# Kernel tuning notes

Measured on AMD Instinct MI355X. Metric: run time of the kernel, lower is better.

Reference implementation:

```python
import jax, jax.numpy as jnp
import numpy as np

C_IN = 128      # pair channel
C_HID = 32      # per-head hidden dim
H = 4           # heads
INF = 1e9
LN_EPS = 1e-5


def setup_inputs() -> dict:
    key = jax.random.key(0)
    ks = jax.random.split(key, 8)
    B, N = 1, 256
    s = 0.02
    return {
        "x": jax.random.normal(ks[0], (B, N, N, C_IN), dtype=jnp.float32),
        "mask": jnp.ones((B, N, N), dtype=jnp.float32),
        "ln_w": jnp.ones((C_IN,), dtype=jnp.float32),
        "ln_b": jnp.zeros((C_IN,), dtype=jnp.float32),
        "w_b": jax.random.normal(ks[1], (H, C_IN), dtype=jnp.float32) * s,      # triangle-bias linear (no bias)
        "w_q": jax.random.normal(ks[2], (H * C_HID, C_IN), dtype=jnp.float32) * s,
        "w_k": jax.random.normal(ks[3], (H * C_HID, C_IN), dtype=jnp.float32) * s,
        "w_v": jax.random.normal(ks[4], (H * C_HID, C_IN), dtype=jnp.float32) * s,
        "w_g": jax.random.normal(ks[5], (H * C_HID, C_IN), dtype=jnp.float32) * s,
        "b_g": jnp.ones((H * C_HID,), dtype=jnp.float32),
        "w_o": jax.random.normal(ks[6], (C_IN, H * C_HID), dtype=jnp.float32) * s,
        "b_o": jnp.zeros((C_IN,), dtype=jnp.float32),
    }


def reference(x, mask, ln_w, ln_b, w_b, w_q, w_k, w_v, w_g, b_g, w_o, b_o):
    # starting=True -> no transpose
    # LayerNorm over channel dim
    mu = jnp.mean(x, axis=-1, keepdims=True)
    var = jnp.var(x, axis=-1, keepdims=True)
    xn = (x - mu) * jax.lax.rsqrt(var + LN_EPS) * ln_w + ln_b            # [B,I,J,C]

    # mask bias: [B, I, 1, 1, J]
    mask_bias = (INF * (mask - 1.0))[..., :, None, None, :]

    # triangle bias: linear -> [B,I,J,H] -> permute -> [B,H,I,J] -> [B,1,H,I,J]
    tri_bias = jnp.einsum("bijc,hc->bhij", xn, w_b)[:, None]

    # QKV projections, per-head: weights reshaped to [H, D, C]
    Wq = w_q.reshape(H, C_HID, C_IN)
    Wk = w_k.reshape(H, C_HID, C_IN)
    Wv = w_v.reshape(H, C_HID, C_IN)
    scale = 1.0 / np.sqrt(C_HID)
    q = jnp.einsum("bijc,hdc->bihjd", xn, Wq) * scale                    # [B,I,H,J,D]
    k = jnp.einsum("bijc,hdc->bihjd", xn, Wk)
    v = jnp.einsum("bijc,hdc->bihjd", xn, Wv)

    # attention over the J (column) axis of each row i
    a = jnp.einsum("bihqd,bihkd->bihqk", q, k) + mask_bias + tri_bias    # [B,I,H,J,J]
    a = jax.nn.softmax(a, axis=-1)
    o = jnp.einsum("bihqk,bihkd->biqhd", a, v)                           # [B,I,J,H,D]

    # sigmoid gating
    g = jax.nn.sigmoid(jnp.einsum("bijc,ec->bije", xn, w_g) + b_g)       # [B,I,J,H*D]
    o = o.reshape(*o.shape[:-2], H * C_HID) * g

    # output projection
    return jnp.einsum("bije,ce->bijc", o, w_o) + b_o                     # [B,I,J,C_in]
```

## Files before the change

kernel.cpp:

```cpp
#include <hip/hip_runtime.h>

#define N 256
#define C 128
#define H 4
#define D 32
#define NP (N*N)
#define LN_EPS 1e-5f
#define LOG2E 1.4426950408889634f

using f32x4 = __attribute__((ext_vector_type(4))) float;
using bf8   = __attribute__((ext_vector_type(8))) short;

__device__ __forceinline__ float bf2f(ushort u) {
    union { uint u; float f; } v; v.u = ((uint)u) << 16; return v.f;
}
__device__ __forceinline__ ushort f2bf(float f) {
    union { float f; uint u; } v; v.f = f;
    uint u = v.u;
    u += 0x7fffu + ((u >> 16) & 1u);
    return (ushort)(u >> 16);
}
__device__ __forceinline__ ushort f2bf_trunc(float f) {
    union { float f; uint u; } v; v.f = f;
    return (ushort)(v.u >> 16);
}

__global__ __launch_bounds__(256) void prep_weights(
    const float* __restrict__ wq, const float* __restrict__ wk,
    const float* __restrict__ wv, const float* __restrict__ wg,
    const float* __restrict__ wb, const float* __restrict__ wo,
    ushort* __restrict__ Wcat, ushort* __restrict__ Wb, ushort* __restrict__ Wo)
{
    int t = blockIdx.x * 256 + threadIdx.x;
    const float scale = 0.17677669529663689f * LOG2E;
    float v;
    if (t < 16384)       v = wq[t] * scale;
    else if (t < 32768)  v = wk[t - 16384];
    else if (t < 49152)  v = wv[t - 32768];
    else                 v = wg[t - 49152];
    Wcat[t] = f2bf(v);
    if (t < 16384) Wo[t] = f2bf(wo[t]);
    if (t < 512)   Wb[t] = f2bf(wb[t]);
}

__global__ __launch_bounds__(256) void ln_kernel(
    const float* __restrict__ x, const float* __restrict__ lnw,
    const float* __restrict__ lnb, ushort* __restrict__ xn)
{
    int wave = threadIdx.x >> 6, lane = threadIdx.x & 63;
    int p = blockIdx.x * 4 + wave;
    const float* xp = x + (size_t)p * C;
    float a0 = xp[lane], a1 = xp[lane + 64];
    float s = a0 + a1, ss = a0 * a0 + a1 * a1;
    #pragma unroll
    for (int m = 1; m < 64; m <<= 1) {
        s  += __shfl_xor(s, m, 64);
        ss += __shfl_xor(ss, m, 64);
    }
    float mean = s * (1.f / 128.f);
    float var  = ss * (1.f / 128.f) - mean * mean;
    float rstd = rsqrtf(var + LN_EPS);
    ushort* op = xn + (size_t)p * C;
    op[lane]      = f2bf((a0 - mean) * rstd * lnw[lane]      + lnb[lane]);
    op[lane + 64] = f2bf((a1 - mean) * rstd * lnw[lane + 64] + lnb[lane + 64]);
}

__global__ __launch_bounds__(256) void tri_kernel(
    const ushort* __restrict__ xn, const ushort* __restrict__ Wb,
    ushort* __restrict__ tri_p)
{
    __shared__ float wb[512];
    int t = threadIdx.x;
    wb[t]       = bf2f(Wb[t]);
    wb[t + 256] = bf2f(Wb[t + 256]);
    __syncthreads();
    int p = blockIdx.x * 256 + t;
    const ushort* xp = xn + (size_t)p * C;
    float acc0 = 0, acc1 = 0, acc2 = 0, acc3 = 0;
    #pragma unroll
    for (int c8 = 0; c8 < 16; c8++) {
        uint4 pk = ((const uint4*)xp)[c8];
        const ushort* u = (const ushort*)&pk;
        #pragma unroll
        for (int j = 0; j < 8; j++) {
            float xv = bf2f(u[j]);
            int c = c8 * 8 + j;
            acc0 += xv * wb[c];
            acc1 += xv * wb[128 + c];
            acc2 += xv * wb[256 + c];
            acc3 += xv * wb[384 + c];
        }
    }
    int q = p >> 8, k = p & 255;
    int qc = q >> 4, quad = (q >> 2) & 3, r = q & 3;
    int n = k >> 4, lrow = k & 15;
    int lane = quad * 16 + lrow;
    int v = n * 4 + r, j = v >> 3, m = v & 7;
    int base = ((qc * 8 + j) * 64 + lane) * 8 + m;
    tri_p[base]             = f2bf(acc0 * LOG2E);
    tri_p[65536 + base]     = f2bf(acc1 * LOG2E);
    tri_p[2 * 65536 + base] = f2bf(acc2 * LOG2E);
    tri_p[3 * 65536 + base] = f2bf(acc3 * LOG2E);
}

__global__ __launch_bounds__(512, 4) void proj_gemm(
    const ushort* __restrict__ xn, const ushort* __restrict__ Wcat,
    const float* __restrict__ bg,
    ushort* __restrict__ qb, ushort* __restrict__ kb,
    ushort* __restrict__ vbT, ushort* __restrict__ gate)
{
    __shared__ ushort At[128 * 128];
    __shared__ ushort Bt[128 * 128];
    int mt = blockIdx.x;
    int nt = blockIdx.y;
    int t  = threadIdx.x;

    const uint4* Ag = (const uint4*)(xn   + (size_t)mt * 128 * C);
    const uint4* Bg = (const uint4*)(Wcat + (size_t)nt * 128 * C);
    #pragma unroll
    for (int ii = 0; ii < 4; ii++) {
        int idx = t + ii * 512;
        int row = idx >> 4, c8 = idx & 15;
        int sc = row * 16 + (c8 ^ (row & 7));
        ((uint4*)At)[sc] = Ag[idx];
        ((uint4*)Bt)[sc] = Bg[idx];
    }
    __syncthreads();

    int wave = t >> 6, lane = t & 63;
    int lrow = lane & 15, quad = lane >> 4;
    int wr = wave >> 1, wc = wave & 1;

    f32x4 acc[2][4];
    #pragma unroll
    for (int mi = 0; mi < 2; mi++)
        #pragma unroll
        for (int ni = 0; ni < 4; ni++) acc[mi][ni] = (f32x4){0.f, 0.f, 0.f, 0.f};

    #pragma unroll
    for (int ks = 0; ks < 4; ks++) {
        int c8 = ks * 4 + quad;
        bf8 a[2], b[4];
        #pragma unroll
        for (int mi = 0; mi < 2; mi++) {
            int row = wr * 32 + mi * 16 + lrow;
            a[mi] = *(const bf8*)&At[(row * 16 + (c8 ^ (row & 7))) * 8];
        }
        #pragma unroll
        for (int ni = 0; ni < 4; ni++) {
            int row = wc * 64 + ni * 16 + lrow;
            b[ni] = *(const bf8*)&Bt[(row * 16 + (c8 ^ (row & 7))) * 8];
        }
        #pragma unroll
        for (int mi = 0; mi < 2; mi++)
            #pragma unroll
            for (int ni = 0; ni < 4; ni++)
                acc[mi][ni] = __builtin_amdgcn_mfma_f32_16x16x32_bf16(a[mi], b[ni], acc[mi][ni], 0, 0, 0);
    }

    if (nt == 2) {
        __syncthreads();
        #pragma unroll
        for (int mi = 0; mi < 2; mi++) {
            #pragma unroll
            for (int ni = 0; ni < 4; ni++) {
                int col = wc * 64 + ni * 16 + lrow;
                #pragma unroll
                for (int r = 0; r < 4; r++) {
                    int keyl = wr * 32 + mi * 16 + quad * 4 + r;
                    Bt[col * 128 + (keyl ^ (lrow << 3))] = f2bf(acc[mi][ni][r]);
                }
            }
        }
        __syncthreads();
        int i_row = mt >> 1;
        #pragma unroll
        for (int itr = 0; itr < 4; itr++) {
            int oidx = itr * 512 + t;
            int col = oidx >> 4, kc = oidx & 15;
            bf8 val = *(const bf8*)&Bt[col * 128 + ((kc * 8) ^ ((col & 15) << 3))];
            *(bf8*)&vbT[(size_t)(i_row * 128 + col) * N + (mt & 1) * 128 + kc * 8] = val;
        }
    } else {
        ushort* dst = (nt == 0) ? qb : (nt == 1) ? kb : gate;
        bool gated = (nt == 3);
        #pragma unroll
        for (int mi = 0; mi < 2; mi++) {
            #pragma unroll
            for (int ni = 0; ni < 4; ni++) {
                int col = wc * 64 + ni * 16 + lrow;
                #pragma unroll
                for (int r = 0; r < 4; r++) {
                    int row = mt * 128 + wr * 32 + mi * 16 + quad * 4 + r;
                    float v = acc[mi][ni][r];
                    if (gated) v = 1.f / (1.f + __expf(-(v + bg[col])));
                    dst[(size_t)row * C + col] = f2bf(v);
                }
            }
        }
    }
}

__global__ __launch_bounds__(512, 4) void attn_kernel(
    const ushort* __restrict__ qb, const ushort* __restrict__ kb,
    const ushort* __restrict__ vbT, const ushort* __restrict__ tri_p,
    const float* __restrict__ mask, ushort* __restrict__ ob)
{
    __shared__ ushort Kf[8192];
    __shared__ ushort Vf[8192];
    __shared__ ushort Pf[8][2048];

    int i  = blockIdx.x;
    int h  = blockIdx.y;
    int t  = threadIdx.x;
    int wave = t >> 6, lane = t & 63;
    int lrow = lane & 15, quad = lane >> 4;

    {
        const ushort* kt = kb + (size_t)(i * N) * C + h * D;
        #pragma unroll
        for (int it = 0; it < 2; it++) {
            int idx = it * 512 + t;
            int key = idx >> 2, d0 = (idx & 3) * 8;
            bf8 kv = *(const bf8*)(kt + (size_t)key * C + d0);
            int c = (idx >> 6) * 64 + (idx & 3) * 16 + ((idx >> 2) & 15);
            *(bf8*)&Kf[c * 8] = kv;
        }
    }
    {
        const ushort* vt = vbT + (size_t)((i * H + h) * D) * N;
        #pragma unroll
        for (int it = 0; it < 2; it++) {
            int idx = it * 512 + t;
            bf8 vv = *(const bf8*)(vt + idx * 8);
            int c = (idx >> 9) * 512 + ((idx >> 2) & 7) * 64 + (idx & 3) * 16 + ((idx >> 5) & 15);
            c ^= (c >> 6) & 7;
            *(bf8*)&Vf[c * 8] = vv;
        }
    }
    float mb[16];
    #pragma unroll
    for (int n = 0; n < 16; n++)
        mb[n] = (1e9f * LOG2E) * (mask[i * N + n * 16 + lrow] - 1.0f);
    __syncthreads();

    ushort* Pw = &Pf[wave][0];
    const ushort* trih = tri_p + (size_t)h * 65536;
    int pq = quad * 32 + (lrow & 7);
    int l3 = (lrow >> 3) & 1;

    #pragma unroll 1
    for (int cc = 0; cc < 2; cc++) {
        int qc = wave * 2 + cc;
        bf8 aq = *(const bf8*)(qb + (size_t)(i * N + qc * 16 + lrow) * C + h * D + quad * 8);
        float sum[4] = {0.f, 0.f, 0.f, 0.f};
        f32x4 o[2];
        o[0] = (f32x4){0.f, 0.f, 0.f, 0.f};
        o[1] = (f32x4){0.f, 0.f, 0.f, 0.f};

        #pragma unroll
        for (int half = 0; half < 2; half++) {
            f32x4 s8[8];
            #pragma unroll
            for (int n8 = 0; n8 < 8; n8++) {
                bf8 kf = *(const bf8*)&Kf[((half * 8 + n8) * 64 + lane) * 8];
                s8[n8] = __builtin_amdgcn_mfma_f32_16x16x32_bf16(
                    aq, kf, (f32x4){0.f, 0.f, 0.f, 0.f}, 0, 0, 0);
            }
            const ushort* tp = trih + ((size_t)(qc * 8 + half * 4) * 64 + lane) * 8;
            bf8 tf[4];
            #pragma unroll
            for (int jj = 0; jj < 4; jj++)
                tf[jj] = *(const bf8*)(tp + jj * 512);

            #pragma unroll
            for (int n8 = 0; n8 < 8; n8++) {
                int pa = (n8 >> 1) * 512 + (((n8 << 1) + l3) & 3) * 128 + pq;
                #pragma unroll
                for (int r = 0; r < 4; r++) {
                    float tb = bf2f(((const ushort*)&tf[n8 >> 1])[((n8 & 1) << 2) + r]);
                    float e  = exp2f(s8[n8][r] + tb + mb[half * 8 + n8]);
                    sum[r]  += e;
                    Pw[pa + r * 8] = f2bf_trunc(e);
                }
            }
            __asm__ volatile("s_waitcnt lgkmcnt(0)" ::: "memory");

            #pragma unroll
            for (int ks = 0; ks < 4; ks++) {
                bf8 ap = *(const bf8*)&Pw[(ks * 64 + lane) * 8];
                int ksg = half * 4 + ks;
                #pragma unroll
                for (int nv = 0; nv < 2; nv++) {
                    int c = nv * 512 + ksg * 64 + (lane ^ (ksg & 7));
                    bf8 bv = *(const bf8*)&Vf[c * 8];
                    o[nv] = __builtin_amdgcn_mfma_f32_16x16x32_bf16(ap, bv, o[nv], 0, 0, 0);
                }
            }
        }
        #pragma unroll
        for (int r = 0; r < 4; r++) {
            float s = sum[r];
            s += __shfl_xor(s, 1, 64);
            s += __shfl_xor(s, 2, 64);
            s += __shfl_xor(s, 4, 64);
            s += __shfl_xor(s, 8, 64);
            sum[r] = 1.f / s;
        }
        #pragma unroll
        for (int nv = 0; nv < 2; nv++) {
            int d = nv * 16 + lrow;
            #pragma unroll
            for (int r = 0; r < 4; r++) {
                int qg = qc * 16 + quad * 4 + r;
                ob[(size_t)(i * N + qg) * C + h * D + d] = f2bf(o[nv][r] * sum[r]);
            }
        }
    }
}

__global__ __launch_bounds__(512, 4) void out_gemm(
    const ushort* __restrict__ ob, const ushort* __restrict__ gate,
    const ushort* __restrict__ Wo, const float* __restrict__ bo,
    float* __restrict__ out)
{
    __shared__ ushort At[128 * 128];
    __shared__ ushort Bt[128 * 128];
    int mt = blockIdx.x;
    int t  = threadIdx.x;

    const uint4* Og = (const uint4*)(ob   + (size_t)mt * 128 * C);
    const uint4* Gg = (const uint4*)(gate + (size_t)mt * 128 * C);
    const uint4* Bg = (const uint4*)Wo;
    #pragma unroll
    for (int ii = 0; ii < 4; ii++) {
        int idx = t + ii * 512;
        int row = idx >> 4, c8 = idx & 15;
        int sc = row * 16 + (c8 ^ (row & 7));
        uint4 o4 = Og[idx], g4 = Gg[idx], r4;
        const ushort* os = (const ushort*)&o4;
        const ushort* gs = (const ushort*)&g4;
        ushort* rs = (ushort*)&r4;
        #pragma unroll
        for (int j = 0; j < 8; j++) rs[j] = f2bf(bf2f(os[j]) * bf2f(gs[j]));
        ((uint4*)At)[sc] = r4;
        ((uint4*)Bt)[sc] = Bg[idx];
    }
    __syncthreads();

    int wave = t >> 6, lane = t & 63;
    int lrow = lane & 15, quad = lane >> 4;
    int wr = wave >> 1, wc = wave & 1;

    f32x4 acc[2][4];
    #pragma unroll
    for (int mi = 0; mi < 2; mi++)
        #pragma unroll
        for (int ni = 0; ni < 4; ni++) acc[mi][ni] = (f32x4){0.f, 0.f, 0.f, 0.f};

    #pragma unroll
    for (int ks = 0; ks < 4; ks++) {
        int c8 = ks * 4 + quad;
        bf8 a[2], b[4];
        #pragma unroll
        for (int mi = 0; mi < 2; mi++) {
            int row = wr * 32 + mi * 16 + lrow;
            a[mi] = *(const bf8*)&At[(row * 16 + (c8 ^ (row & 7))) * 8];
        }
        #pragma unroll
        for (int ni = 0; ni < 4; ni++) {
            int row = wc * 64 + ni * 16 + lrow;
            b[ni] = *(const bf8*)&Bt[(row * 16 + (c8 ^ (row & 7))) * 8];
        }
        #pragma unroll
        for (int mi = 0; mi < 2; mi++)
            #pragma unroll
            for (int ni = 0; ni < 4; ni++)
                acc[mi][ni] = __builtin_amdgcn_mfma_f32_16x16x32_bf16(a[mi], b[ni], acc[mi][ni], 0, 0, 0);
    }

    #pragma unroll
    for (int mi = 0; mi < 2; mi++) {
        #pragma unroll
        for (int ni = 0; ni < 4; ni++) {
            int col = wc * 64 + ni * 16 + lrow;
            float bias = bo[col];
            #pragma unroll
            for (int r = 0; r < 4; r++) {
                int row = mt * 128 + wr * 32 + mi * 16 + quad * 4 + r;
                out[(size_t)row * C + col] = acc[mi][ni][r] + bias;
            }
        }
    }
}

extern "C" void kernel_launch(void* const* d_in, const int* in_sizes, int n_in,
                              void* d_out, int out_size, void* d_ws, size_t ws_size,
                              hipStream_t stream)
{
    const float* x    = (const float*)d_in[0];
    const float* mask = (const float*)d_in[1];
    const float* lnw  = (const float*)d_in[2];
    const float* lnb  = (const float*)d_in[3];
    const float* wb   = (const float*)d_in[4];
    const float* wq   = (const float*)d_in[5];
    const float* wk   = (const float*)d_in[6];
    const float* wv   = (const float*)d_in[7];
    const float* wg   = (const float*)d_in[8];
    const float* bg   = (const float*)d_in[9];
    const float* wo   = (const float*)d_in[10];
    const float* bo   = (const float*)d_in[11];
    float* out = (float*)d_out;

    uintptr_t w = (uintptr_t)d_ws;
    ushort* xn    = (ushort*)w; w += (size_t)NP * C * 2;
    ushort* qb    = (ushort*)w; w += (size_t)NP * C * 2;
    ushort* kb    = (ushort*)w; w += (size_t)NP * C * 2;
    ushort* vbT   = (ushort*)w; w += (size_t)NP * C * 2;
    ushort* gate  = (ushort*)w; w += (size_t)NP * C * 2;
    ushort* ob    = (ushort*)w; w += (size_t)NP * C * 2;
    ushort* tri_p = (ushort*)w; w += (size_t)H * NP * 2;
    ushort* Wcat  = (ushort*)w; w += 512 * 128 * 2;
    ushort* Wb    = (ushort*)w; w += 512 * 2;
    ushort* Wo    = (ushort*)w; w += 128 * 128 * 2;

    prep_weights<<<256, 256, 0, stream>>>(wq, wk, wv, wg, wb, wo, Wcat, Wb, Wo);
    ln_kernel<<<NP / 4, 256, 0, stream>>>(x, lnw, lnb, xn);
    tri_kernel<<<NP / 256, 256, 0, stream>>>(xn, Wb, tri_p);
    proj_gemm<<<dim3(NP / 128, 4), 512, 0, stream>>>(xn, Wcat, bg, qb, kb, vbT, gate);
    attn_kernel<<<dim3(N, H), 512, 0, stream>>>(qb, kb, vbT, tri_p, mask, ob);
    out_gemm<<<NP / 128, 512, 0, stream>>>(ob, gate, Wo, bo, out);
}
```

Baseline: 181.7 us.

## Fuse LayerNorm into tri-bias and projection GEMM kernels, drop xn buffer

Removes the standalone LayerNorm and triangle-bias kernels and the bf16 xn intermediate. One kernel recomputes LayerNorm and produces the tri bias with a wave reduction. The projection GEMM now recomputes LayerNorm from fp32 x into shared memory and loops over all four weight tiles per block, so the A tile is reused instead of being reloaded by four blocks. In exchange, x is read twice in fp32 instead of once plus a bf16 reread, the grid shrinks from 2048 to 512 blocks, and the four N tiles run serially inside each block.

```diff
diff --git a/kernel.cpp b/kernel.cpp
--- a/kernel.cpp
+++ b/kernel.cpp
@@ -28,8 +28,8 @@
 __global__ __launch_bounds__(256) void prep_weights(
     const float* __restrict__ wq, const float* __restrict__ wk,
     const float* __restrict__ wv, const float* __restrict__ wg,
-    const float* __restrict__ wb, const float* __restrict__ wo,
-    ushort* __restrict__ Wcat, ushort* __restrict__ Wb, ushort* __restrict__ Wo)
+    const float* __restrict__ wo,
+    ushort* __restrict__ Wcat, ushort* __restrict__ Wo)
 {
     int t = blockIdx.x * 256 + threadIdx.x;
     const float scale = 0.17677669529663689f * LOG2E;
@@ -40,12 +40,12 @@
     else                 v = wg[t - 49152];
     Wcat[t] = f2bf(v);
     if (t < 16384) Wo[t] = f2bf(wo[t]);
-    if (t < 512)   Wb[t] = f2bf(wb[t]);
-}
-
-__global__ __launch_bounds__(256) void ln_kernel(
+}
+
+__global__ __launch_bounds__(256) void ln_tri_kernel(
     const float* __restrict__ x, const float* __restrict__ lnw,
-    const float* __restrict__ lnb, ushort* __restrict__ xn)
+    const float* __restrict__ lnb, const float* __restrict__ wb,
+    ushort* __restrict__ tri_p)
 {
     int wave = threadIdx.x >> 6, lane = threadIdx.x & 63;
     int p = blockIdx.x * 4 + wave;
@@ -60,51 +60,34 @@
     float mean = s * (1.f / 128.f);
     float var  = ss * (1.f / 128.f) - mean * mean;
     float rstd = rsqrtf(var + LN_EPS);
-    ushort* op = xn + (size_t)p * C;
-    op[lane]      = f2bf((a0 - mean) * rstd * lnw[lane]      + lnb[lane]);
-    op[lane + 64] = f2bf((a1 - mean) * rstd * lnw[lane + 64] + lnb[lane + 64]);
-}
-
-__global__ __launch_bounds__(256) void tri_kernel(
-    const ushort* __restrict__ xn, const ushort* __restrict__ Wb,
-    ushort* __restrict__ tri_p)
-{
-    __shared__ float wb[512];
-    int t = threadIdx.x;
-    wb[t]       = bf2f(Wb[t]);
-    wb[t + 256] = bf2f(Wb[t + 256]);
-    __syncthreads();
-    int p = blockIdx.x * 256 + t;
-    const ushort* xp = xn + (size_t)p * C;
-    float acc0 = 0, acc1 = 0, acc2 = 0, acc3 = 0;
-    #pragma unroll
-    for (int c8 = 0; c8 < 16; c8++) {
-        uint4 pk = ((const uint4*)xp)[c8];
-        const ushort* u = (const ushort*)&pk;
-        #pragma unroll
-        for (int j = 0; j < 8; j++) {
-            float xv = bf2f(u[j]);
-            int c = c8 * 8 + j;
-            acc0 += xv * wb[c];
-            acc1 += xv * wb[128 + c];
-            acc2 += xv * wb[256 + c];
-            acc3 += xv * wb[384 + c];
-        }
-    }
-    int q = p >> 8, k = p & 255;
-    int qc = q >> 4, quad = (q >> 2) & 3, r = q & 3;
-    int n = k >> 4, lrow = k & 15;
-    int lane = quad * 16 + lrow;
-    int v = n * 4 + r, j = v >> 3, m = v & 7;
-    int base = ((qc * 8 + j) * 64 + lane) * 8 + m;
-    tri_p[base]             = f2bf(acc0 * LOG2E);
-    tri_p[65536 + base]     = f2bf(acc1 * LOG2E);
-    tri_p[2 * 65536 + base] = f2bf(acc2 * LOG2E);
-    tri_p[3 * 65536 + base] = f2bf(acc3 * LOG2E);
-}
-
-__global__ __launch_bounds__(512, 4) void proj_gemm(
-    const ushort* __restrict__ xn, const ushort* __restrict__ Wcat,
+    float v0 = (a0 - mean) * rstd * lnw[lane]      + lnb[lane];
+    float v1 = (a1 - mean) * rstd * lnw[lane + 64] + lnb[lane + 64];
+
+    float t[H];
+    #pragma unroll
+    for (int h = 0; h < H; h++)
+        t[h] = v0 * wb[h * C + lane] + v1 * wb[h * C + 64 + lane];
+    #pragma unroll
+    for (int m = 1; m < 64; m <<= 1) {
+        #pragma unroll
+        for (int h = 0; h < H; h++) t[h] += __shfl_xor(t[h], m, 64);
+    }
+    if (lane == 0) {
+        int q = p >> 8, k = p & 255;
+        int qc = q >> 4, quad = (q >> 2) & 3, r = q & 3;
+        int n = k >> 4, lrow = k & 15;
+        int ln2 = quad * 16 + lrow;
+        int v = n * 4 + r, j = v >> 3, m = v & 7;
+        int base = ((qc * 8 + j) * 64 + ln2) * 8 + m;
+        #pragma unroll
+        for (int h = 0; h < H; h++)
+            tri_p[h * 65536 + base] = f2bf(t[h] * LOG2E);
+    }
+}
+
+__global__ __launch_bounds__(512, 4) void proj_ln_gemm(
+    const float* __restrict__ x, const float* __restrict__ lnw,
+    const float* __restrict__ lnb, const ushort* __restrict__ Wcat,
     const float* __restrict__ bg,
     ushort* __restrict__ qb, ushort* __restrict__ kb,
     ushort* __restrict__ vbT, ushort* __restrict__ gate)
@@ -112,89 +95,123 @@
     __shared__ ushort At[128 * 128];
     __shared__ ushort Bt[128 * 128];
     int mt = blockIdx.x;
-    int nt = blockIdx.y;
     int t  = threadIdx.x;
 
-    const uint4* Ag = (const uint4*)(xn   + (size_t)mt * 128 * C);
-    const uint4* Bg = (const uint4*)(Wcat + (size_t)nt * 128 * C);
     #pragma unroll
     for (int ii = 0; ii < 4; ii++) {
         int idx = t + ii * 512;
         int row = idx >> 4, c8 = idx & 15;
-        int sc = row * 16 + (c8 ^ (row & 7));
-        ((uint4*)At)[sc] = Ag[idx];
-        ((uint4*)Bt)[sc] = Bg[idx];
-    }
-    __syncthreads();
+        const float* xr = x + ((size_t)(mt * 128 + row)) * C + c8 * 8;
+        float4 f0 = ((const float4*)xr)[0];
+        float4 f1 = ((const float4*)xr)[1];
+        float s  = f0.x + f0.y + f0.z + f0.w + f1.x + f1.y + f1.z + f1.w;
+        float ss = f0.x*f0.x + f0.y*f0.y + f0.z*f0.z + f0.w*f0.w
+                 + f1.x*f1.x + f1.y*f1.y + f1.z*f1.z + f1.w*f1.w;
+        #pragma unroll
+        for (int m = 1; m < 16; m <<= 1) {
+            s  += __shfl_xor(s, m, 64);
+            ss += __shfl_xor(ss, m, 64);
+        }
+        float mean = s * (1.f / 128.f);
+        float var  = ss * (1.f / 128.f) - mean * mean;
+        float rstd = rsqrtf(var + LN_EPS);
+        float4 w0 = ((const float4*)(lnw + c8 * 8))[0];
+        float4 w1 = ((const float4*)(lnw + c8 * 8))[1];
+        float4 b0 = ((const float4*)(lnb + c8 * 8))[0];
+        float4 b1 = ((const float4*)(lnb + c8 * 8))[1];
+        union { ushort us[8]; uint4 v; } r;
+        r.us[0] = f2bf((f0.x - mean) * rstd * w0.x + b0.x);
+        r.us[1] = f2bf((f0.y - mean) * rstd * w0.y + b0.y);
+        r.us[2] = f2bf((f0.z - mean) * rstd * w0.z + b0.z);
+        r.us[3] = f2bf((f0.w - mean) * rstd * w0.w + b0.w);
+        r.us[4] = f2bf((f1.x - mean) * rstd * w1.x + b1.x);
+        r.us[5] = f2bf((f1.y - mean) * rstd * w1.y + b1.y);
+        r.us[6] = f2bf((f1.z - mean) * rstd * w1.z + b1.z);
+        r.us[7] = f2bf((f1.w - mean) * rstd * w1.w + b1.w);
+        ((uint4*)At)[row * 16 + (c8 ^ (row & 7))] = r.v;
+    }
 
     int wave = t >> 6, lane = t & 63;
     int lrow = lane & 15, quad = lane >> 4;
     int wr = wave >> 1, wc = wave & 1;
-
-    f32x4 acc[2][4];
-    #pragma unroll
-    for (int mi = 0; mi < 2; mi++)
-        #pragma unroll
-        for (int ni = 0; ni < 4; ni++) acc[mi][ni] = (f32x4){0.f, 0.f, 0.f, 0.f};
-
-    #pragma unroll
-    for (int ks = 0; ks < 4; ks++) {
-        int c8 = ks * 4 + quad;
-        bf8 a[2], b[4];
-        #pragma unroll
-        for (int mi = 0; mi < 2; mi++) {
-            int row = wr * 32 + mi * 16 + lrow;
-            a[mi] = *(const bf8*)&At[(row * 16 + (c8 ^ (row & 7))) * 8];
-        }
-        #pragma unroll
-        for (int ni = 0; ni < 4; ni++) {
-            int row = wc * 64 + ni * 16 + lrow;
-            b[ni] = *(const bf8*)&Bt[(row * 16 + (c8 ^ (row & 7))) * 8];
-        }
+    int i_row = mt >> 1;
+
+    #pragma unroll 1
+    for (int nt = 0; nt < 4; nt++) {
+        __syncthreads();
+        const uint4* Bg = (const uint4*)(Wcat + (size_t)nt * 128 * C);
+        #pragma unroll
+        for (int ii = 0; ii < 4; ii++) {
+            int idx = t + ii * 512;
+            int row = idx >> 4, c8 = idx & 15;
+            ((uint4*)Bt)[row * 16 + (c8 ^ (row & 7))] = Bg[idx];
+        }
+        __syncthreads();
+
+        f32x4 acc[2][4];
         #pragma unroll
         for (int mi = 0; mi < 2; mi++)
             #pragma unroll
-            for (int ni = 0; ni < 4; ni++)
-                acc[mi][ni] = __builtin_amdgcn_mfma_f32_16x16x32_bf16(a[mi], b[ni], acc[mi][ni], 0, 0, 0);
-    }
-
-    if (nt == 2) {
-        __syncthreads();
-        #pragma unroll
-        for (int mi = 0; mi < 2; mi++) {
+            for (int ni = 0; ni < 4; ni++) acc[mi][ni] = (f32x4){0.f, 0.f, 0.f, 0.f};
+
+        #pragma unroll
+        for (int ks = 0; ks < 4; ks++) {
+            int c8 = ks * 4 + quad;
+            bf8 a[2], b[4];
+            #pragma unroll
+            for (int mi = 0; mi < 2; mi++) {
+                int row = wr * 32 + mi * 16 + lrow;
+                a[mi] = *(const bf8*)&At[(row * 16 + (c8 ^ (row & 7))) * 8];
+            }
             #pragma unroll
             for (int ni = 0; ni < 4; ni++) {
-                int col = wc * 64 + ni * 16 + lrow;
+                int row = wc * 64 + ni * 16 + lrow;
+                b[ni] = *(const bf8*)&Bt[(row * 16 + (c8 ^ (row & 7))) * 8];
+            }
+            #pragma unroll
+            for (int mi = 0; mi < 2; mi++)
                 #pragma unroll
-                for (int r = 0; r < 4; r++) {
-                    int keyl = wr * 32 + mi * 16 + quad * 4 + r;
-                    Bt[col * 128 + (keyl ^ (lrow << 3))] = f2bf(acc[mi][ni][r]);
+                for (int ni = 0; ni < 4; ni++)
+                    acc[mi][ni] = __builtin_amdgcn_mfma_f32_16x16x32_bf16(a[mi], b[ni], acc[mi][ni], 0, 0, 0);
+        }
+
+        if (nt == 2) {
+            __syncthreads();
+            #pragma unroll
+            for (int mi = 0; mi < 2; mi++) {
+                #pragma unroll
+                for (int ni = 0; ni < 4; ni++) {
+                    int col = wc * 64 + ni * 16 + lrow;
+                    #pragma unroll
+                    for (int r = 0; r < 4; r++) {
+                        int keyl = wr * 32 + mi * 16 + quad * 4 + r;
+                        Bt[col * 128 + (keyl ^ (lrow << 3))] = f2bf(acc[mi][ni][r]);
+                    }
                 }
             }
-        }
-        __syncthreads();
-        int i_row = mt >> 1;
-        #pragma unroll
-        for (int itr = 0; itr < 4; itr++) {
-            int oidx = itr * 512 + t;
-            int col = oidx >> 4, kc = oidx & 15;
-            bf8 val = *(const bf8*)&Bt[col * 128 + ((kc * 8) ^ ((col & 15) << 3))];
-            *(bf8*)&vbT[(size_t)(i_row * 128 + col) * N + (mt & 1) * 128 + kc * 8] = val;
-        }
-    } else {
-        ushort* dst = (nt == 0) ? qb : (nt == 1) ? kb : gate;
-        bool gated = (nt == 3);
-        #pragma unroll
-        for (int mi = 0; mi < 2; mi++) {
-            #pragma unroll
-            for (int ni = 0; ni < 4; ni++) {
-                int col = wc * 64 + ni * 16 + lrow;
+            __syncthreads();
+            #pragma unroll
+            for (int itr = 0; itr < 4; itr++) {
+                int oidx = itr * 512 + t;
+                int col = oidx >> 4, kc = oidx & 15;
+                bf8 val = *(const bf8*)&Bt[col * 128 + ((kc * 8) ^ ((col & 15) << 3))];
+                *(bf8*)&vbT[(size_t)(i_row * 128 + col) * N + (mt & 1) * 128 + kc * 8] = val;
+            }
+        } else {
+            ushort* dst = (nt == 0) ? qb : (nt == 1) ? kb : gate;
+            bool gated = (nt == 3);
+            #pragma unroll
+            for (int mi = 0; mi < 2; mi++) {
                 #pragma unroll
-                for (int r = 0; r < 4; r++) {
-                    int row = mt * 128 + wr * 32 + mi * 16 + quad * 4 + r;
-                    float v = acc[mi][ni][r];
-                    if (gated) v = 1.f / (1.f + __expf(-(v + bg[col])));
-                    dst[(size_t)row * C + col] = f2bf(v);
+                for (int ni = 0; ni < 4; ni++) {
+                    int col = wc * 64 + ni * 16 + lrow;
+                    #pragma unroll
+                    for (int r = 0; r < 4; r++) {
+                        int row = mt * 128 + wr * 32 + mi * 16 + quad * 4 + r;
+                        float v = acc[mi][ni][r];
+                        if (gated) v = 1.f / (1.f + __expf(-(v + bg[col])));
+                        dst[(size_t)row * C + col] = f2bf(v);
+                    }
                 }
             }
         }
@@ -413,7 +430,6 @@
     float* out = (float*)d_out;
 
     uintptr_t w = (uintptr_t)d_ws;
-    ushort* xn    = (ushort*)w; w += (size_t)NP * C * 2;
     ushort* qb    = (ushort*)w; w += (size_t)NP * C * 2;
     ushort* kb    = (ushort*)w; w += (size_t)NP * C * 2;
     ushort* vbT   = (ushort*)w; w += (size_t)NP * C * 2;
@@ -421,13 +437,11 @@
     ushort* ob    = (ushort*)w; w += (size_t)NP * C * 2;
     ushort* tri_p = (ushort*)w; w += (size_t)H * NP * 2;
     ushort* Wcat  = (ushort*)w; w += 512 * 128 * 2;
-    ushort* Wb    = (ushort*)w; w += 512 * 2;
     ushort* Wo    = (ushort*)w; w += 128 * 128 * 2;
 
-    prep_weights<<<256, 256, 0, stream>>>(wq, wk, wv, wg, wb, wo, Wcat, Wb, Wo);
-    ln_kernel<<<NP / 4, 256, 0, stream>>>(x, lnw, lnb, xn);
-    tri_kernel<<<NP / 256, 256, 0, stream>>>(xn, Wb, tri_p);
-    proj_gemm<<<dim3(NP / 128, 4), 512, 0, stream>>>(xn, Wcat, bg, qb, kb, vbT, gate);
+    prep_weights<<<256, 256, 0, stream>>>(wq, wk, wv, wg, wo, Wcat, Wo);
+    ln_tri_kernel<<<NP / 4, 256, 0, stream>>>(x, lnw, lnb, wb, tri_p);
+    proj_ln_gemm<<<512, 512, 0, stream>>>(x, lnw, lnb, Wcat, bg, qb, kb, vbT, gate);
     attn_kernel<<<dim3(N, H), 512, 0, stream>>>(qb, kb, vbT, tri_p, mask, ob);
     out_gemm<<<NP / 128, 512, 0, stream>>>(ob, gate, Wo, bo, out);
 }
```

Result: slower. 191.1 us (+5.2%).
